# Optimization experiments

Hardware: AMD Instinct MI355X
Metric: run time of the kernel (lower is better)

Reference implementation:

```python
import jax, jax.numpy as jnp
import numpy as np

HIDDEN = 768
HEADS = 12
DK = 64
DV = 64

def setup_inputs() -> dict:
    key = jax.random.key(0)
    k1, k2, k3, k4, k5, k6 = jax.random.split(key, 6)
    B, N = 4, 2048
    x = jax.random.normal(k1, (B, HIDDEN, N), dtype=jnp.float32)
    mask = jax.random.randint(k2, (B, N), 0, 2, dtype=jnp.int32)
    # xavier_uniform for Linear(hidden -> d): limit = sqrt(6/(hidden+d))
    def xavier(k, out_d, in_d, lead=()):
        lim = float(np.sqrt(6.0 / (in_d + out_d)))
        return jax.random.uniform(k, lead + (out_d, in_d), jnp.float32, -lim, lim)
    Wq = xavier(k3, DK, HIDDEN, (HEADS,))   # (H, d_k, hidden)
    Wk = xavier(k4, DK, HIDDEN, (HEADS,))
    Wv = xavier(k5, DV, HIDDEN, (HEADS,))
    Wo = xavier(k6, HIDDEN, HEADS * DV)     # (hidden, H*d_v)
    return {"x": x, "Wq": Wq, "Wk": Wk, "Wv": Wv, "Wo": Wo, "mask": mask}

def reference(x, Wq, Wk, Wv, Wo, mask):
    # x: (B, hidden, N) -> (B, N, hidden)
    xt = jnp.transpose(x, (0, 2, 1))
    q = jnp.einsum('bnc,hdc->bhnd', xt, Wq)  # (B,H,N,d_k)
    k = jnp.einsum('bnc,hdc->bhnd', xt, Wk)
    v = jnp.einsum('bnc,hdc->bhnd', xt, Wv)  # (B,H,N,d_v)
    scale = 1.0 / jnp.sqrt(jnp.asarray(DK, x.dtype))
    qk = jnp.einsum('bhnd,bhmd->bhnm', q, k) * scale  # (B,H,N,N)
    neg_inf = jnp.asarray(-jnp.inf, x.dtype)
    qk = jnp.where(mask[:, None, None, :] != 0, qk, neg_inf)  # mask key positions
    attn = jax.nn.softmax(qk, axis=-1)
    ctx = jnp.einsum('bhnm,bhmd->bhnd', attn, v)  # (B,H,N,d_v)
    B, H, N, D = ctx.shape
    combined = jnp.transpose(ctx, (0, 2, 1, 3)).reshape(B, N, H * D)  # cat over heads
    out = jnp.einsum('bnf,cf->bnc', combined, Wo)  # Linear(H*d_v -> hidden)
    return jnp.transpose(out, (0, 2, 1))  # (B, hidden, N)
```

## Files before the change

kernel.cpp:

```cpp
#include <hip/hip_runtime.h>

typedef _Float16 f16;
typedef __attribute__((ext_vector_type(8))) _Float16 f16x8;
typedef __attribute__((ext_vector_type(4))) _Float16 f16x4;
typedef __attribute__((ext_vector_type(2))) _Float16 f16x2;
typedef __attribute__((ext_vector_type(4))) float f32x4;

#define DEVINL __device__ __forceinline__

DEVINL void gload16(const void* g, void* l) {
  __builtin_amdgcn_global_load_lds(
      (const __attribute__((address_space(1))) void*)g,
      (__attribute__((address_space(3))) void*)l, 16, 0, 0);
}

DEVINL f32x4 mfma16(f16x8 a, f16x8 b, f32x4 c) {
  return __builtin_amdgcn_mfma_f32_16x16x32_f16(a, b, c, 0, 0, 0);
}

DEVINL f16x2 cvt_pk(float a, float b) {
  return __builtin_bit_cast(f16x2, __builtin_amdgcn_cvt_pkrtz(a, b));
}

__global__ __launch_bounds__(256) void convert_w(const float* __restrict__ wq,
                                                 const float* __restrict__ wk,
                                                 const float* __restrict__ wv,
                                                 const float* __restrict__ wo,
                                                 f16* __restrict__ wcat,
                                                 f16* __restrict__ wob) {
  int seg = blockIdx.x / 576;
  int i = ((blockIdx.x % 576) * 256 + threadIdx.x) * 4;
  const float* src = seg == 0 ? wq : (seg == 1 ? wk : (seg == 2 ? wv : wo));
  f16* dst = seg < 3 ? wcat + seg * 589824 : wob;
  f32x4 v = *(const f32x4*)(src + i);
  f16x4 o = {(f16)v[0], (f16)v[1], (f16)v[2], (f16)v[3]};
  *(f16x4*)(dst + i) = o;
}

__global__ __launch_bounds__(256) void transpose_x(const float* __restrict__ x,
                                                   f16* __restrict__ xt) {
  __shared__ __attribute__((aligned(16))) f16 T[64 * 66];
  const int b = blockIdx.z, c0 = blockIdx.y * 64, n0 = blockIdx.x * 64;
  const int t = threadIdx.x;
  const float* xb = x + (size_t)b * 768 * 2048;
#pragma unroll
  for (int r = 0; r < 4; ++r) {
    int chunk = r * 256 + t;
    int row = chunk >> 4, c4 = (chunk & 15) * 4;
    f32x4 v = *(const f32x4*)&xb[(size_t)(c0 + row) * 2048 + n0 + c4];
#pragma unroll
    for (int e = 0; e < 4; ++e) T[row * 66 + c4 + e] = (f16)v[e];
  }
  __syncthreads();
  f16* xtb = xt + (size_t)b * 2048 * 768;
  int n = t >> 2, cp = (t & 3) * 16;
  __attribute__((aligned(16))) f16 vals[16];
#pragma unroll
  for (int j = 0; j < 16; ++j) vals[j] = T[(cp + j) * 66 + n];
  *(f16x8*)&xtb[(size_t)(n0 + n) * 768 + c0 + cp] = *(const f16x8*)&vals[0];
  *(f16x8*)&xtb[(size_t)(n0 + n) * 768 + c0 + cp + 8] = *(const f16x8*)&vals[8];
}

__global__ __launch_bounds__(256, 2)
void gemm_kernel(const f16* __restrict__ A, const f16* __restrict__ Bt,
                 f16* __restrict__ qkt, f16* __restrict__ vbuf,
                 float* __restrict__ outp, int kind) {
  constexpr int K = 768;
  const int b = blockIdx.z;
  const int n0 = blockIdx.x * 128;
  const int m0 = blockIdx.y * 128;
  const int t = threadIdx.x;
  const int lane = t & 63, w = t >> 6, g = lane >> 4, lo = lane & 15;
  const int wm = (w >> 1) * 64, wn = (w & 1) * 64;

  __shared__ __attribute__((aligned(16))) f16 smem[16384];
  f16* As = smem;
  f16* Bs = smem + 8192;

  const f16* Ab = A + (size_t)m0 * K;
  const f16* Bb = Bt + (size_t)b * 2048 * K + (size_t)n0 * K;

  const f32x4 zf = {0.f, 0.f, 0.f, 0.f};
  f32x4 acc[4][4];
#pragma unroll
  for (int i = 0; i < 4; ++i)
#pragma unroll
    for (int j = 0; j < 4; ++j) acc[i][j] = zf;

  for (int kt = 0; kt < K; kt += 64) {
    __syncthreads();
#pragma unroll
    for (int r = 0; r < 4; ++r) {
      int chunk = r * 256 + t;
      int row = chunk >> 3;
      int c8 = (chunk & 7) ^ (row & 7);
      gload16(Ab + (size_t)row * K + kt + c8 * 8, As + chunk * 8);
    }
#pragma unroll
    for (int r = 0; r < 4; ++r) {
      int chunk = r * 256 + t;
      int row = chunk >> 3;
      int c8 = (chunk & 7) ^ (row & 7);
      gload16(Bb + (size_t)row * K + kt + c8 * 8, Bs + chunk * 8);
    }
    __syncthreads();
#pragma unroll
    for (int kk = 0; kk < 2; ++kk) {
      f16x8 af[4], bfr[4];
#pragma unroll
      for (int i = 0; i < 4; ++i) {
        int row = wm + i * 16 + lo;
        af[i] = *(const f16x8*)&As[row * 64 + (((kk * 4 + g) ^ (row & 7)) * 8)];
      }
#pragma unroll
      for (int j = 0; j < 4; ++j) {
        int col = wn + j * 16 + lo;
        bfr[j] = *(const f16x8*)&Bs[col * 64 + (((kk * 4 + g) ^ (col & 7)) * 8)];
      }
#pragma unroll
      for (int i = 0; i < 4; ++i)
#pragma unroll
        for (int j = 0; j < 4; ++j)
          acc[i][j] = mfma16(af[i], bfr[j], acc[i][j]);
    }
  }

  if (kind == 1) {
    float* Cb = outp + (size_t)b * 768 * 2048;
#pragma unroll
    for (int i = 0; i < 4; ++i) {
      int row = m0 + wm + i * 16 + g * 4;
#pragma unroll
      for (int j = 0; j < 4; ++j) {
        int col = n0 + wn + j * 16 + lo;
#pragma unroll
        for (int r2 = 0; r2 < 4; ++r2)
          Cb[(size_t)(row + r2) * 2048 + col] = acc[i][j][r2];
      }
    }
  } else if (m0 >= 1536) {
    f16* Vb = vbuf + (size_t)b * 768 * 2048;
#pragma unroll
    for (int i = 0; i < 4; ++i) {
      int row = m0 - 1536 + wm + i * 16 + g * 4;
#pragma unroll
      for (int j = 0; j < 4; ++j) {
        int col = n0 + wn + j * 16 + lo;
#pragma unroll
        for (int r2 = 0; r2 < 4; ++r2)
          Vb[(size_t)(row + r2) * 2048 + col] = (f16)acc[i][j][r2];
      }
    }
  } else {
    __syncthreads();
    f16* T = smem;
#pragma unroll
    for (int i = 0; i < 4; ++i)
#pragma unroll
      for (int j = 0; j < 4; ++j) {
        int nl = wn + j * 16 + lo;
#pragma unroll
        for (int r2 = 0; r2 < 4; ++r2) {
          int ml = wm + i * 16 + g * 4 + r2;
          T[nl * 128 + (((ml >> 3) ^ (nl & 15)) * 8) + (ml & 7)] =
              (f16)acc[i][j][r2];
        }
      }
    __syncthreads();
    f16* Qb = qkt + (size_t)b * 2048 * 1536;
    int n = t >> 1, half = t & 1;
#pragma unroll
    for (int c = 0; c < 8; ++c) {
      int chunk = half * 8 + c;
      f16x8 v = *(const f16x8*)&T[n * 128 + ((chunk ^ (n & 15)) * 8)];
      *(f16x8*)&Qb[(size_t)(n0 + n) * 1536 + m0 + chunk * 8] = v;
    }
  }
}

__global__ __launch_bounds__(256, 3)
void attn_kernel(const f16* __restrict__ qkt, const f16* __restrict__ vbuf,
                 const int* __restrict__ mask, f16* __restrict__ ctxt) {
  const int bh = blockIdx.y;
  const int b = bh / 12, h = bh % 12;
  const int n0 = blockIdx.x * 128;
  const int t = threadIdx.x;
  const int lane = t & 63, w = t >> 6, g = lane >> 4, lo = lane & 15;

  __shared__ __attribute__((aligned(16))) f16 Kd[2][4096];
  __shared__ __attribute__((aligned(16))) f16 Vd[2][4096];
  __shared__ __attribute__((aligned(16))) f16 Ps[4][2048];
  __shared__ __attribute__((aligned(16))) f16 bias_s[2048];

  const f16* qb = qkt + (size_t)b * 2048 * 1536;
  const int* mb = mask + b * 2048;
#pragma unroll
  for (int r = 0; r < 8; ++r) {
    int i = r * 256 + t;
    bias_s[i] = (f16)(mb[i] ? 0.f : -60000.f);
  }

  constexpr float QS = 0.125f * 1.44269504088896f;
  f16x8 qa[2][2];
#pragma unroll
  for (int fm = 0; fm < 2; ++fm)
#pragma unroll
    for (int kk = 0; kk < 2; ++kk) {
      f16x8 v = *(const f16x8*)&qb[(size_t)(n0 + w * 32 + fm * 16 + lo) * 1536 +
                                   h * 64 + kk * 32 + g * 8];
#pragma unroll
      for (int e = 0; e < 8; ++e) v[e] = (f16)((float)v[e] * QS);
      qa[fm][kk] = v;
    }

  const f32x4 zf = {0.f, 0.f, 0.f, 0.f};
  f32x4 oacc[2][4];
  float mrun[2], lrun[2];
#pragma unroll
  for (int fm = 0; fm < 2; ++fm) {
#pragma unroll
    for (int fd = 0; fd < 4; ++fd) oacc[fm][fd] = zf;
    mrun[fm] = -3e38f;
    lrun[fm] = 0.f;
  }

  const f16* kb_g = qb + 768 + h * 64;
  const f16* vb_g = vbuf + (size_t)b * 768 * 2048 + (size_t)(h * 64) * 2048;
  f16* psw = &Ps[w][0];

#define STAGE_KV(BUF, M0)                                                     \
  {                                                                           \
    _Pragma("unroll") for (int r = 0; r < 2; ++r) {                           \
      int chunk = r * 256 + t;                                                \
      int row = chunk >> 3;                                                   \
      int c8 = (chunk & 7) ^ (row & 7);                                       \
      gload16(kb_g + (size_t)((M0) + row) * 1536 + c8 * 8,                    \
              &Kd[BUF][0] + chunk * 8);                                       \
    }                                                                         \
    _Pragma("unroll") for (int r = 0; r < 2; ++r) {                           \
      int chunk = r * 256 + t;                                                \
      int d = chunk >> 3;                                                     \
      int c8 = (chunk & 7) ^ (d & 7);                                         \
      gload16(vb_g + (size_t)d * 2048 + (M0) + c8 * 8, &Vd[BUF][0] + chunk * 8);\
    }                                                                         \
  }

  STAGE_KV(0, 0);
  __syncthreads();

  for (int mt = 0; mt < 32; ++mt) {
    const int cur = mt & 1;
    const int m0 = mt * 64;
    if (mt + 1 < 32) STAGE_KV(cur ^ 1, m0 + 64);

    const f16* Kb = &Kd[cur][0];
    const f16* Vb = &Vd[cur][0];

    f32x4 sacc[2][4];
#pragma unroll
    for (int fn = 0; fn < 4; ++fn) {
      f16x4 b4 = *(const f16x4*)&bias_s[m0 + fn * 16 + g * 4];
      f32x4 ba = {(float)b4[0], (float)b4[1], (float)b4[2], (float)b4[3]};
      sacc[0][fn] = ba;
      sacc[1][fn] = ba;
    }
#pragma unroll
    for (int kk = 0; kk < 2; ++kk)
#pragma unroll
      for (int fn = 0; fn < 4; ++fn) {
        int m = fn * 16 + lo;
        f16x8 kf = *(const f16x8*)&Kb[m * 64 + (((kk * 4 + g) ^ (m & 7)) * 8)];
        sacc[0][fn] = mfma16(kf, qa[0][kk], sacc[0][fn]);
        sacc[1][fn] = mfma16(kf, qa[1][kk], sacc[1][fn]);
      }

    f16x4 p16[2][4];
#pragma unroll
    for (int fm = 0; fm < 2; ++fm) {
      f32x4 vm = sacc[fm][0];
#pragma unroll
      for (int fn = 1; fn < 4; ++fn)
#pragma unroll
        for (int r = 0; r < 4; ++r) vm[r] = fmaxf(vm[r], sacc[fm][fn][r]);
      float mx = fmaxf(fmaxf(vm[0], vm[1]), fmaxf(vm[2], vm[3]));
      mx = fmaxf(mx, __shfl_xor(mx, 16, 64));
      mx = fmaxf(mx, __shfl_xor(mx, 32, 64));
      if (__any(mx > mrun[fm] + 8.f)) {
        float mnew = fmaxf(mrun[fm], mx);
        float alpha = __builtin_amdgcn_exp2f(mrun[fm] - mnew);
        mrun[fm] = mnew;
        lrun[fm] *= alpha;
#pragma unroll
        for (int fd = 0; fd < 4; ++fd) oacc[fm][fd] *= alpha;
      }
      float mcur = mrun[fm];
      f32x4 vs_ = zf;
#pragma unroll
      for (int fn = 0; fn < 4; ++fn) {
        f32x4 pv;
#pragma unroll
        for (int r = 0; r < 4; ++r)
          pv[r] = __builtin_amdgcn_exp2f(sacc[fm][fn][r] - mcur);
        vs_ += pv;
        f16x2 plo = cvt_pk(pv[0], pv[1]);
        f16x2 phi = cvt_pk(pv[2], pv[3]);
        f16x4 ph = {plo[0], plo[1], phi[0], phi[1]};
        p16[fm][fn] = ph;
      }
      float rs = (vs_[0] + vs_[1]) + (vs_[2] + vs_[3]);
      rs += __shfl_xor(rs, 16, 64);
      rs += __shfl_xor(rs, 32, 64);
      lrun[fm] += rs;
    }

#pragma unroll
    for (int fm = 0; fm < 2; ++fm) {
      int q32 = fm * 16 + lo;
      int sw = q32 & 7;
#pragma unroll
      for (int fn = 0; fn < 4; ++fn) {
        int cq = fn * 2 + (g >> 1);
        *(f16x4*)&psw[q32 * 64 + ((cq ^ sw) * 8) + (g & 1) * 4] = p16[fm][fn];
      }
    }
#pragma unroll
    for (int kk = 0; kk < 2; ++kk) {
      f16x8 pa[2], vf[4];
#pragma unroll
      for (int fm = 0; fm < 2; ++fm) {
        int q32 = fm * 16 + lo;
        pa[fm] =
            *(const f16x8*)&psw[q32 * 64 + (((kk * 4 + g) ^ (q32 & 7)) * 8)];
      }
#pragma unroll
      for (int fd = 0; fd < 4; ++fd) {
        int d = fd * 16 + lo;
        vf[fd] = *(const f16x8*)&Vb[d * 64 + (((kk * 4 + g) ^ (d & 7)) * 8)];
      }
#pragma unroll
      for (int fm = 0; fm < 2; ++fm)
#pragma unroll
        for (int fd = 0; fd < 4; ++fd)
          oacc[fm][fd] = mfma16(vf[fd], pa[fm], oacc[fm][fd]);
    }

    __syncthreads();
  }

  f16* T2 = &Kd[0][0];
#pragma unroll
  for (int fm = 0; fm < 2; ++fm) {
    float rcp = 1.f / lrun[fm];
    int q = w * 32 + fm * 16 + lo;
    int sw = q & 7;
#pragma unroll
    for (int fd = 0; fd < 4; ++fd) {
      int c8 = fd * 2 + (g >> 1);
      f16x4 o4 = {(f16)(oacc[fm][fd][0] * rcp), (f16)(oacc[fm][fd][1] * rcp),
                  (f16)(oacc[fm][fd][2] * rcp), (f16)(oacc[fm][fd][3] * rcp)};
      *(f16x4*)&T2[q * 64 + ((c8 ^ sw) * 8) + (g & 1) * 4] = o4;
    }
  }
  __syncthreads();
  f16* cb = ctxt + (size_t)b * 2048 * 768;
  int qrow = t >> 1, half = t & 1;
#pragma unroll
  for (int c = 0; c < 4; ++c) {
    int c8 = half * 4 + c;
    f16x8 v = *(const f16x8*)&T2[qrow * 64 + ((c8 ^ (qrow & 7)) * 8)];
    *(f16x8*)&cb[(size_t)(n0 + qrow) * 768 + h * 64 + c8 * 8] = v;
  }
#undef STAGE_KV
}

extern "C" void kernel_launch(void* const* d_in, const int* in_sizes, int n_in,
                              void* d_out, int out_size, void* d_ws,
                              size_t ws_size, hipStream_t stream) {
  const float* x  = (const float*)d_in[0];
  const float* Wq = (const float*)d_in[1];
  const float* Wk = (const float*)d_in[2];
  const float* Wv = (const float*)d_in[3];
  const float* Wo = (const float*)d_in[4];
  const int* mask = (const int*)d_in[5];
  float* out = (float*)d_out;

  f16* Xt   = (f16*)d_ws;
  f16* Wcat = Xt + 6291456;
  f16* Wob  = Wcat + 1769472;
  f16* QKt  = Wob + 589824;
  f16* Vbuf = QKt + 12582912;
  f16* Ctxt = Xt;

  convert_w<<<2304, 256, 0, stream>>>(Wq, Wk, Wv, Wo, Wcat, Wob);
  transpose_x<<<dim3(32, 12, 4), 256, 0, stream>>>(x, Xt);
  gemm_kernel<<<dim3(16, 18, 4), 256, 0, stream>>>(Wcat, Xt, QKt, Vbuf, nullptr, 0);
  attn_kernel<<<dim3(16, 48), 256, 0, stream>>>(QKt, Vbuf, mask, Ctxt);
  gemm_kernel<<<dim3(16, 6, 4), 256, 0, stream>>>(Wob, Ctxt, nullptr, nullptr, out, 1);
}
```

Measured before the change: 231.1 us.

## Split output GEMM into smaller-tile kernel and unroll attention KV double-buffer loop

Moves the output projection out of the shared GEMM kernel into a dedicated gemm_out with 128x64 tiles, which doubles the block count (384 to 768) to fill more CUs and allows 3 blocks per CU. The attention loop is manually unrolled by two with fixed buffer indices and pointer increments instead of computed offsets. This removes the runtime kind branch and cur-index arithmetic. The cost is more A-tile reloads in the output GEMM and larger code size in the attention kernel.

```diff
diff --git a/kernel.cpp b/kernel.cpp
--- a/kernel.cpp
+++ b/kernel.cpp
@@ -63,8 +63,7 @@
 
 __global__ __launch_bounds__(256, 2)
 void gemm_kernel(const f16* __restrict__ A, const f16* __restrict__ Bt,
-                 f16* __restrict__ qkt, f16* __restrict__ vbuf,
-                 float* __restrict__ outp, int kind) {
+                 f16* __restrict__ qkt, f16* __restrict__ vbuf) {
   constexpr int K = 768;
   const int b = blockIdx.z;
   const int n0 = blockIdx.x * 128;
@@ -125,20 +124,7 @@
     }
   }
 
-  if (kind == 1) {
-    float* Cb = outp + (size_t)b * 768 * 2048;
-#pragma unroll
-    for (int i = 0; i < 4; ++i) {
-      int row = m0 + wm + i * 16 + g * 4;
-#pragma unroll
-      for (int j = 0; j < 4; ++j) {
-        int col = n0 + wn + j * 16 + lo;
-#pragma unroll
-        for (int r2 = 0; r2 < 4; ++r2)
-          Cb[(size_t)(row + r2) * 2048 + col] = acc[i][j][r2];
-      }
-    }
-  } else if (m0 >= 1536) {
+  if (m0 >= 1536) {
     f16* Vb = vbuf + (size_t)b * 768 * 2048;
 #pragma unroll
     for (int i = 0; i < 4; ++i) {
@@ -174,6 +160,83 @@
       int chunk = half * 8 + c;
       f16x8 v = *(const f16x8*)&T[n * 128 + ((chunk ^ (n & 15)) * 8)];
       *(f16x8*)&Qb[(size_t)(n0 + n) * 1536 + m0 + chunk * 8] = v;
+    }
+  }
+}
+
+__global__ __launch_bounds__(256, 3)
+void gemm_out(const f16* __restrict__ A, const f16* __restrict__ Bt,
+              float* __restrict__ outp) {
+  constexpr int K = 768;
+  const int b = blockIdx.z;
+  const int n0 = blockIdx.x * 64;
+  const int m0 = blockIdx.y * 128;
+  const int t = threadIdx.x;
+  const int lane = t & 63, w = t >> 6, g = lane >> 4, lo = lane & 15;
+  const int wm = (w >> 1) * 64, wn = (w & 1) * 32;
+
+  __shared__ __attribute__((aligned(16))) f16 smem[12288];
+  f16* As = smem;
+  f16* Bs = smem + 8192;
+
+  const f16* Ab = A + (size_t)m0 * K;
+  const f16* Bb = Bt + (size_t)b * 2048 * K + (size_t)n0 * K;
+
+  const f32x4 zf = {0.f, 0.f, 0.f, 0.f};
+  f32x4 acc[4][2];
+#pragma unroll
+  for (int i = 0; i < 4; ++i)
+#pragma unroll
+    for (int j = 0; j < 2; ++j) acc[i][j] = zf;
+
+  for (int kt = 0; kt < K; kt += 64) {
+    __syncthreads();
+#pragma unroll
+    for (int r = 0; r < 4; ++r) {
+      int chunk = r * 256 + t;
+      int row = chunk >> 3;
+      int c8 = (chunk & 7) ^ (row & 7);
+      gload16(Ab + (size_t)row * K + kt + c8 * 8, As + chunk * 8);
+    }
+#pragma unroll
+    for (int r = 0; r < 2; ++r) {
+      int chunk = r * 256 + t;
+      int row = chunk >> 3;
+      int c8 = (chunk & 7) ^ (row & 7);
+      gload16(Bb + (size_t)row * K + kt + c8 * 8, Bs + chunk * 8);
+    }
+    __syncthreads();
+#pragma unroll
+    for (int kk = 0; kk < 2; ++kk) {
+      f16x8 af[4], bfr[2];
+#pragma unroll
+      for (int i = 0; i < 4; ++i) {
+        int row = wm + i * 16 + lo;
+        af[i] = *(const f16x8*)&As[row * 64 + (((kk * 4 + g) ^ (row & 7)) * 8)];
+      }
+#pragma unroll
+      for (int j = 0; j < 2; ++j) {
+        int col = wn + j * 16 + lo;
+        bfr[j] = *(const f16x8*)&Bs[col * 64 + (((kk * 4 + g) ^ (col & 7)) * 8)];
+      }
+#pragma unroll
+      for (int i = 0; i < 4; ++i)
+#pragma unroll
+        for (int j = 0; j < 2; ++j)
+          acc[i][j] = mfma16(af[i], bfr[j], acc[i][j]);
+    }
+  }
+
+  float* Cb = outp + (size_t)b * 768 * 2048;
+#pragma unroll
+  for (int i = 0; i < 4; ++i) {
+    int row = m0 + wm + i * 16 + g * 4;
+#pragma unroll
+    for (int j = 0; j < 2; ++j) {
+      int col = n0 + wn + j * 16 + lo;
+#pragma unroll
+      for (int r2 = 0; r2 < 4; ++r2)
+        Cb[(size_t)(row + r2) * 2048 + col] = acc[i][j][r2];
     }
   }
 }
@@ -228,34 +291,24 @@
   const f16* vb_g = vbuf + (size_t)b * 768 * 2048 + (size_t)(h * 64) * 2048;
   f16* psw = &Ps[w][0];
 
-#define STAGE_KV(BUF, M0)                                                     \
+#define STAGE_KV(BUF, KP, VP)                                                 \
   {                                                                           \
     _Pragma("unroll") for (int r = 0; r < 2; ++r) {                           \
       int chunk = r * 256 + t;                                                \
       int row = chunk >> 3;                                                   \
       int c8 = (chunk & 7) ^ (row & 7);                                       \
-      gload16(kb_g + (size_t)((M0) + row) * 1536 + c8 * 8,                    \
-              &Kd[BUF][0] + chunk * 8);                                       \
+      gload16((KP) + (size_t)row * 1536 + c8 * 8, &Kd[BUF][0] + chunk * 8);   \
     }                                                                         \
     _Pragma("unroll") for (int r = 0; r < 2; ++r) {                           \
       int chunk = r * 256 + t;                                                \
       int d = chunk >> 3;                                                     \
       int c8 = (chunk & 7) ^ (d & 7);                                         \
-      gload16(vb_g + (size_t)d * 2048 + (M0) + c8 * 8, &Vd[BUF][0] + chunk * 8);\
+      gload16((VP) + (size_t)d * 2048 + c8 * 8, &Vd[BUF][0] + chunk * 8);     \
     }                                                                         \
   }
 
-  STAGE_KV(0, 0);
-  __syncthreads();
-
-  for (int mt = 0; mt < 32; ++mt) {
-    const int cur = mt & 1;
-    const int m0 = mt * 64;
-    if (mt + 1 < 32) STAGE_KV(cur ^ 1, m0 + 64);
-
-    const f16* Kb = &Kd[cur][0];
-    const f16* Vb = &Vd[cur][0];
-
+  auto tile_body = [&](const f16* __restrict__ Kb, const f16* __restrict__ Vb,
+                       int m0) {
     f32x4 sacc[2][4];
 #pragma unroll
     for (int fn = 0; fn < 4; ++fn) {
@@ -343,7 +396,26 @@
         for (int fd = 0; fd < 4; ++fd)
           oacc[fm][fd] = mfma16(vf[fd], pa[fm], oacc[fm][fd]);
     }
-
+  };
+
+  STAGE_KV(0, kb_g, vb_g);
+  const f16* kn = kb_g + 64 * 1536;
+  const f16* vn = vb_g + 64;
+  __syncthreads();
+
+#pragma unroll 1
+  for (int mt2 = 0; mt2 < 16; ++mt2) {
+    STAGE_KV(1, kn, vn);
+    kn += 64 * 1536;
+    vn += 64;
+    tile_body(&Kd[0][0], &Vd[0][0], mt2 * 128);
+    __syncthreads();
+    if (mt2 < 15) {
+      STAGE_KV(0, kn, vn);
+      kn += 64 * 1536;
+      vn += 64;
+    }
+    tile_body(&Kd[1][0], &Vd[1][0], mt2 * 128 + 64);
     __syncthreads();
   }
 
@@ -393,7 +465,7 @@
 
   convert_w<<<2304, 256, 0, stream>>>(Wq, Wk, Wv, Wo, Wcat, Wob);
   transpose_x<<<dim3(32, 12, 4), 256, 0, stream>>>(x, Xt);
-  gemm_kernel<<<dim3(16, 18, 4), 256, 0, stream>>>(Wcat, Xt, QKt, Vbuf, nullptr, 0);
+  gemm_kernel<<<dim3(16, 18, 4), 256, 0, stream>>>(Wcat, Xt, QKt, Vbuf);
   attn_kernel<<<dim3(16, 48), 256, 0, stream>>>(QKt, Vbuf, mask, Ctxt);
-  gemm_kernel<<<dim3(16, 6, 4), 256, 0, stream>>>(Wob, Ctxt, nullptr, nullptr, out, 1);
-}
+  gemm_out<<<dim3(32, 6, 4), 256, 0, stream>>>(Wob, Ctxt, out);
+}
```

Result: slower. 235.9 us (+2.1%).
